# Kernel tuning notes

Hardware: AMD Instinct MI355X
Metric: run time of the kernel (lower is better)

The kernel has to match this reference:

```python
import jax, jax.numpy as jnp
import numpy as np

DILATIONS = (1, 3, 5)
NUM_HEADS = 2


def _conv(x, w, b, dil=1, pad=0):
    # x: [B,C,H,W], w: [O,I,kh,kw] (OIHW), 'same'-style padding = dilation for k=3
    y = jax.lax.conv_general_dilated(
        x, w, window_strides=(1, 1), padding=[(pad, pad), (pad, pad)],
        rhs_dilation=(dil, dil), dimension_numbers=('NCHW', 'OIHW', 'NCHW'))
    return y + b[None, :, None, None]


def setup_inputs() -> dict:
    key = jax.random.key(0)
    ks = jax.random.split(key, 4)
    B, Cin, H, W = 4, 256, 64, 64
    Cout = 256
    x = jax.random.normal(ks[0], (B, Cin, H, W), dtype=jnp.float32)
    # kaiming-uniform-like init scale
    q_w = jax.random.uniform(ks[1], (Cout, Cin, 3, 3), dtype=jnp.float32,
                             minval=-1.0, maxval=1.0) * np.sqrt(6.0 / (Cin * 9))
    k_w = jax.random.uniform(ks[2], (Cout, Cin, 1, 1), dtype=jnp.float32,
                             minval=-1.0, maxval=1.0) * np.sqrt(6.0 / Cin)
    v_w = jax.random.uniform(ks[3], (Cout, Cin, 1, 1), dtype=jnp.float32,
                             minval=-1.0, maxval=1.0) * np.sqrt(6.0 / Cin)
    q_b = jnp.zeros((Cout,), jnp.float32)
    k_b = jnp.zeros((Cout,), jnp.float32)
    v_b = jnp.zeros((Cout,), jnp.float32)
    return {"x": x, "q_w": q_w, "q_b": q_b, "k_w": k_w, "k_b": k_b,
            "v_w": v_w, "v_b": v_b}


def reference(x, q_w, q_b, k_w, k_b, v_w, v_b):
    B, C, H, W = x.shape
    Cout = q_w.shape[0]
    hd = Cout // NUM_HEADS  # head_dim
    # ds_conv2d: sum of SiLU(dilated conv) over dilations 1,3,5 (padding=dilation)
    q = sum(jax.nn.silu(_conv(x, q_w, q_b, dil=d, pad=d)) for d in DILATIONS)
    k = _conv(x, k_w, k_b)
    v = _conv(x, v_w, v_b)
    N = H * W
    # [B, heads, head_dim, N]
    q = q.reshape(B, NUM_HEADS, hd, N)
    k = k.reshape(B, NUM_HEADS, hd, N)
    v = v.reshape(B, NUM_HEADS, hd, N)
    # energy[b,h,n,m] = sum_d q[b,h,d,n] * k[b,h,d,m]
    energy = jnp.einsum('bhdn,bhdm->bhnm', q, k)
    attn = jax.nn.softmax(energy / jnp.sqrt(jnp.float32(hd)), axis=-1)
    # out[b,h,n,d] = sum_m attn[b,h,n,m] * v[b,h,d,m]; then back to [B,C,H,W]
    out = jnp.einsum('bhnm,bhdm->bhdn', attn, v)
    return out.reshape(B, Cout, H, W)
```

## Files before the change

### kernel.cpp

```cpp
#include <hip/hip_runtime.h>
#include <cstdint>

typedef __attribute__((ext_vector_type(8))) _Float16 f16x8;
typedef __attribute__((ext_vector_type(4))) float f32x4;

#define DEV static __device__ __forceinline__

DEV void gld_lds16(void* lds_base, const void* gsrc) {
  __builtin_amdgcn_global_load_lds(
      (const __attribute__((address_space(1))) unsigned int*)gsrc,
      (__attribute__((address_space(3))) unsigned int*)lds_base,
      16, 0, 0);
}
DEV unsigned short f2h(float f) {
  _Float16 h = (_Float16)f;
  return __builtin_bit_cast(unsigned short, h);
}
DEV float h2f(unsigned short u) {
  _Float16 h = __builtin_bit_cast(_Float16, u);
  return (float)h;
}
DEV unsigned pk2h(float a, float b) {
  auto h2 = __builtin_amdgcn_cvt_pkrtz(a, b);
  return __builtin_bit_cast(unsigned, h2);
}
DEV float v_exp2(float x) { float r; asm("v_exp_f32 %0, %1" : "=v"(r) : "v"(x)); return r; }
DEV float v_rcp(float x) { float r; asm("v_rcp_f32 %0, %1" : "=v"(r) : "v"(x)); return r; }


__global__ __launch_bounds__(256) void k_prep_x(const float* __restrict__ x, char* __restrict__ xpad) {
  __shared__ float xs[32 * 257];
  int h = blockIdx.x, b = blockIdx.y, t = threadIdx.x;
  const float* xb = x + (size_t)b * 1048576 + h * 64;
  for (int half = 0; half < 2; half++) {
    int w0 = half * 32;
    for (int kk = 0; kk < 32; kk++) {
      int flat = kk * 256 + t;
      int ci = flat >> 5, w = flat & 31;
      xs[w * 257 + ci] = xb[ci * 4096 + w0 + w];
    }
    __syncthreads();
    for (int g = 0; g < 4; g++) {
      int w = g * 8 + (t >> 5);
      int cg = t & 31;
      float v0 = xs[w * 257 + cg * 8 + 0], v1 = xs[w * 257 + cg * 8 + 1];
      float v2 = xs[w * 257 + cg * 8 + 2], v3 = xs[w * 257 + cg * 8 + 3];
      float v4 = xs[w * 257 + cg * 8 + 4], v5 = xs[w * 257 + cg * 8 + 5];
      float v6 = xs[w * 257 + cg * 8 + 6], v7 = xs[w * 257 + cg * 8 + 7];
      uint4 pk;
      pk.x = pk2h(v0, v1);
      pk.y = pk2h(v2, v3);
      pk.z = pk2h(v4, v5);
      pk.w = pk2h(v6, v7);
      *(uint4*)(xpad + ((size_t)((b * 74 + h + 5) * 74) + w0 + w + 5) * 512 + cg * 16) = pk;
    }
    __syncthreads();
  }
}

__global__ __launch_bounds__(256) void k_prep_w(
    const float* __restrict__ qw, const float* __restrict__ kw, const float* __restrict__ vw,
    unsigned short* __restrict__ Wq, unsigned short* __restrict__ Wk, unsigned short* __restrict__ Wv) {
  int gid = blockIdx.x * 256 + threadIdx.x;
  const float* q9 = qw + (size_t)gid * 9;
#pragma unroll
  for (int tp = 0; tp < 9; tp++) Wq[tp * 65536 + gid] = f2h(q9[tp]);
  Wk[gid] = f2h(kw[gid]);
  Wv[gid] = f2h(vw[gid]);
}

__global__ __launch_bounds__(256, 2) void k_conv_kv(
    const char* __restrict__ xpad, const unsigned short* __restrict__ Wk,
    const unsigned short* __restrict__ Wv, const float* __restrict__ kb,
    const float* __restrict__ vb, unsigned short* __restrict__ K, unsigned short* __restrict__ V) {
  __shared__ char sm[32768];
  char* Xs = sm;
  char* Ws = sm + 16384;
  int t = threadIdx.x, lane = t & 63, wid = t >> 6, q4 = lane >> 4, l15 = lane & 15;
  int px0 = blockIdx.x * 128;
  int b = px0 >> 12, nn = px0 & 4095;
  int h = blockIdx.y;
  int mode = blockIdx.z;
  int co0 = h * 128;
  const char* Wsrc = (const char*)(mode ? Wv : Wk);
  int wm = wid & 1, wn = wid >> 1;
  f32x4 acc[4][4] = {};
  for (int c = 0; c < 4; c++) {
    __syncthreads();
    for (int ch = wid * 1024; ch < 16384; ch += 4096) {
      int o = ch + lane * 16;
      int r = o >> 7;
      int n = nn + r, hh = n >> 6, ww2 = n & 63;
      int col = (o & 127) ^ ((r & 7) << 4);
      gld_lds16(Xs + ch, xpad + ((size_t)((b * 74 + hh + 5) * 74) + ww2 + 5) * 512 + c * 128 + col);
    }
    for (int ch = wid * 1024; ch < 16384; ch += 4096) {
      int o = ch + lane * 16;
      int r = o >> 7;
      int col = (o & 127) ^ ((r & 7) << 4);
      gld_lds16(Ws + ch, Wsrc + (co0 + r) * 512 + c * 128 + col);
    }
    asm volatile("s_waitcnt vmcnt(0)" ::: "memory");
    __syncthreads();
    int xg = mode ? wn : wm;
    int wg = mode ? wm : wn;
#pragma unroll
    for (int kt = 0; kt < 2; kt++) {
      f16x8 xf[4], wf[4];
#pragma unroll
      for (int i = 0; i < 4; i++) {
        int rx = xg * 64 + i * 16 + l15;
        xf[i] = *(const f16x8*)(Xs + ((rx * 128 + kt * 64 + q4 * 16) ^ ((rx & 7) << 4)));
        int rw = wg * 64 + i * 16 + l15;
        wf[i] = *(const f16x8*)(Ws + ((rw * 128 + kt * 64 + q4 * 16) ^ ((rw & 7) << 4)));
      }
#pragma unroll
      for (int m = 0; m < 4; m++)
#pragma unroll
        for (int n = 0; n < 4; n++)
          acc[m][n] = mode ? __builtin_amdgcn_mfma_f32_16x16x32_f16(wf[m], xf[n], acc[m][n], 0, 0, 0)
                           : __builtin_amdgcn_mfma_f32_16x16x32_f16(xf[m], wf[n], acc[m][n], 0, 0, 0);
    }
  }
  int bh = b * 2 + h;
  if (mode == 0) {
#pragma unroll
    for (int m = 0; m < 4; m++)
#pragma unroll
      for (int n = 0; n < 4; n++) {
        int dd = wn * 64 + n * 16 + l15;
        float bias = kb[co0 + dd];
#pragma unroll
        for (int j = 0; j < 4; j++) {
          int npix = nn + wm * 64 + m * 16 + q4 * 4 + j;
          K[(size_t)(bh * 4096 + npix) * 128 + dd] = f2h(acc[m][n][j] + bias);
        }
      }
  } else {
#pragma unroll
    for (int m = 0; m < 4; m++)
#pragma unroll
      for (int j = 0; j < 4; j++) {
        int cr = wm * 64 + m * 16 + q4 * 4 + j;
        float bias = vb[co0 + cr];
#pragma unroll
        for (int n = 0; n < 4; n++) {
          int pc = nn + wn * 64 + (n >> 1) * 32 + (l15 >> 2) * 8 + (n & 1) * 4 + (l15 & 3);
          V[(size_t)(bh * 128 + cr) * 4096 + pc] = f2h(acc[m][n][j] + bias);
        }
      }
  }
}

__global__ __launch_bounds__(512, 2) void k_conv_q(
    const char* __restrict__ xpad, const unsigned short* __restrict__ Wq,
    const float* __restrict__ qb, unsigned short* __restrict__ Q) {
  extern __shared__ char sm[];
  char* As = sm + 32768;
  int t = threadIdx.x, lane = t & 63, wid = t >> 6, q4 = lane >> 4, l15 = lane & 15;
  int fblk = blockIdx.x;
  int g = (fblk & 7) * 32 + (fblk >> 3);
  int h2 = g & 31, b = (g >> 5) & 3, ch2 = g >> 7;
  int h0 = h2 * 2;
  int co0 = ch2 * 128;
  int wn = wid & 1, wq = wid >> 1;
  int hr = wq >> 1, wloc = wq & 1;
  const int dil[3] = {1, 3, 5};
  const char* WqB = (const char*)Wq;
  f32x4 accd[3][2][4] = {};

#define STAGE_B(dstbuf, kh_, c_, kw_)                                             \
  {                                                                               \
    const char* src_ = WqB + (size_t)((kh_)*3 + (kw_)) * 131072 + co0 * 512 + (c_)*128; \
    char* dst_ = (dstbuf);                                                        \
    for (int ch = wid * 1024; ch < 16384; ch += 8192) {                           \
      int o = ch + lane * 16;                                                     \
      int r = o >> 7;                                                             \
      int col = (o & 127) ^ ((r & 7) << 4);                                       \
      gld_lds16(dst_ + ch, src_ + r * 512 + col);                                 \
    }                                                                             \
  }

#define STAGE_A_ROW(slot_, pr_, c_)                                               \
  {                                                                               \
    const char* src_ = xpad + ((size_t)(b * 74 + (pr_)) * 74) * 512 + (c_)*128;   \
    char* dst_ = As + (slot_)*9472;                                               \
    for (int ch = wid * 1024; ch < 9472; ch += 8192) {                            \
      int o = ch + lane * 16;                                                     \
      if (o < 9472) {                                                             \
        int r = o >> 7;                                                           \
        int col = (o & 127) ^ ((r & 7) << 4);                                     \
        gld_lds16(dst_ + ch, src_ + r * 512 + col);                               \
      }                                                                           \
    }                                                                             \
  }

#define STAGE_A(kh_, c_)                                                          \
  {                                                                               \
    if ((kh_) == 1) {                                                             \
      for (int s = 0; s < 2; s++) STAGE_A_ROW(s, h0 + s + 5, c_);                 \
    } else {                                                                      \
      for (int di = 0; di < 3; di++)                                              \
        for (int s = 0; s < 2; s++)                                               \
          STAGE_A_ROW(di * 2 + s, h0 + s + ((kh_)-1) * dil[di] + 5, c_);          \
    }                                                                             \
  }

  STAGE_A(0, 0);
  STAGE_B(sm, 0, 0, 0);
  asm volatile("s_waitcnt vmcnt(0)" ::: "memory");
  __syncthreads();

  int cur = 0;
  for (int kh = 0; kh < 3; kh++) {
    for (int c = 0; c < 4; c++) {
      for (int kw = 0; kw < 3; kw++) {
        int kwn = kw + 1, cn = c, khn = kh;
        if (kwn == 3) { kwn = 0; cn = c + 1; if (cn == 4) { cn = 0; khn = kh + 1; } }
        char* Bnext = cur ? sm : sm + 16384;
        if (khn < 3) STAGE_B(Bnext, khn, cn, kwn);
        const char* Bc = cur ? sm + 16384 : sm;
        f16x8 bf[4][2];
#pragma unroll
        for (int n = 0; n < 4; n++)
#pragma unroll
          for (int kt = 0; kt < 2; kt++) {
            int rc = wn * 64 + n * 16 + l15;
            bf[n][kt] = *(const f16x8*)(Bc + ((rc * 128 + kt * 64 + q4 * 16) ^ ((rc & 7) << 4)));
          }
#pragma unroll
        for (int di = 0; di < 3; di++) {
          int dw = (kw - 1) * dil[di] + 5;
          const char* Ad = As + (kh == 1 ? hr : di * 2 + hr) * 9472;
          f16x8 af[2][2];
#pragma unroll
          for (int m = 0; m < 2; m++)
#pragma unroll
            for (int kt = 0; kt < 2; kt++) {
              int wp = wloc * 32 + m * 16 + l15 + dw;
              af[m][kt] = *(const f16x8*)(Ad + ((wp * 128 + kt * 64 + q4 * 16) ^ ((wp & 7) << 4)));
            }
          __builtin_amdgcn_s_setprio(1);
#pragma unroll
          for (int m = 0; m < 2; m++)
#pragma unroll
            for (int n = 0; n < 4; n++)
#pragma unroll
              for (int kt = 0; kt < 2; kt++)
                accd[di][m][n] = __builtin_amdgcn_mfma_f32_16x16x32_f16(af[m][kt], bf[n][kt], accd[di][m][n], 0, 0, 0);
          __builtin_amdgcn_s_setprio(0);
        }
        asm volatile("s_waitcnt vmcnt(0)" ::: "memory");
        __syncthreads();
        cur ^= 1;
      }
      int cn2 = c + 1, khn2 = kh;
      if (cn2 == 4) { cn2 = 0; khn2 = kh + 1; }
      if (khn2 < 3) {
        STAGE_A(khn2, cn2);
        asm volatile("s_waitcnt vmcnt(0)" ::: "memory");
        __syncthreads();
      }
    }
  }
#undef STAGE_A
#undef STAGE_A_ROW
#undef STAGE_B
  const float LOG2E = 1.4426950408889634f;
  const float QSCALE = 0.12751879523176862f;
#pragma unroll
  for (int n = 0; n < 4; n++) {
    float bias = qb[co0 + wn * 64 + n * 16 + l15];
#pragma unroll
    for (int m = 0; m < 2; m++)
#pragma unroll
      for (int j = 0; j < 4; j++) {
        float s = 0.f;
#pragma unroll
        for (int di = 0; di < 3; di++) {
          float v = accd[di][m][n][j] + bias;
          s += v * v_rcp(1.0f + v_exp2(-v * LOG2E));
        }
        int w = wloc * 32 + m * 16 + q4 * 4 + j;
        int npix = (h0 + hr) * 64 + w;
        int dd = wn * 64 + n * 16 + l15;
        Q[((size_t)(b * 2 + ch2) * 4096 + npix) * 128 + dd] = f2h(s * QSCALE);
      }
  }
}

__global__ __launch_bounds__(256, 2) void k_attn(
    const unsigned short* __restrict__ Q, const unsigned short* __restrict__ K,
    const unsigned short* __restrict__ V, float* __restrict__ out,
    unsigned short* __restrict__ o1buf, float* __restrict__ mlbuf) {
  __shared__ char sm[65536];
  int t = threadIdx.x, lane = t & 63, wid = t >> 6, q4 = lane >> 4, l15 = lane & 15;
  int fblk = blockIdx.x;
  int g = (fblk & 7) * 64 + (fblk >> 3);
  int nb = g & 31, bh = (g >> 5) & 7, half = g >> 8;
  int b = bh >> 1, hh = bh & 1;
  int n0 = nb * 128;
  const char* Qg = (const char*)(Q + ((size_t)bh * 4096 + n0) * 128);
  const char* Kg = (const char*)(K + (size_t)bh * 4096 * 128) + half * 524288;
  const char* Vg = (const char*)(V + (size_t)bh * 128 * 4096) + half * 4096;
  f16x8 qf[2][4];
#pragma unroll
  for (int nt = 0; nt < 2; nt++)
#pragma unroll
    for (int kt = 0; kt < 4; kt++) {
      int rn = wid * 32 + nt * 16 + l15;
      qf[nt][kt] = *(const f16x8*)(Qg + (size_t)rn * 256 + kt * 64 + q4 * 16);
    }
  const char* pT0 = sm + (((l15 * 256 + 0 * 64 + q4 * 16) ^ (l15 << 4)));
  const char* pT1 = sm + (((l15 * 256 + 1 * 64 + q4 * 16) ^ (l15 << 4)));
  const char* pT2 = sm + (((l15 * 256 + 2 * 64 + q4 * 16) ^ (l15 << 4)));
  const char* pT3 = sm + (((l15 * 256 + 3 * 64 + q4 * 16) ^ (l15 << 4)));
  const char* pU0 = sm + 32768 + (((l15 * 128 + 0 * 64 + q4 * 16) ^ ((l15 & 7) << 4)));
  const char* pU1 = sm + 32768 + (((l15 * 128 + 1 * 64 + q4 * 16) ^ ((l15 & 7) << 4)));
  int ks[4], vs[4], lch[4];
#pragma unroll
  for (int c2 = 0; c2 < 4; c2++) {
    int ch = wid * 1024 + c2 * 4096;
    int o = ch + lane * 16;
    lch[c2] = ch;
    ks[c2] = o ^ (((o >> 8) & 15) << 4);
    int dd = o >> 7;
    vs[c2] = dd * 8192 + ((o & 127) ^ ((dd & 7) << 4));
  }
#pragma unroll
  for (int c2 = 0; c2 < 4; c2++) gld_lds16(sm + lch[c2], Kg + ks[c2]);
#pragma unroll
  for (int c2 = 0; c2 < 4; c2++) gld_lds16(sm + 32768 + lch[c2], Vg + vs[c2]);
  asm volatile("s_waitcnt vmcnt(0)" ::: "memory");
  __syncthreads();
  f32x4 Ofr[8][2] = {};
  float mrun[2] = {-3e38f, -3e38f};
  float lrun[2] = {0.f, 0.f};
  const char* kgp = Kg;
  const char* vgp = Vg;

#define ATTN_ITER(KB, VB, KBN, VBN, do_pf)                                          \
  {                                                                                 \
    if (do_pf) {                                                                    \
      kgp += 16384;                                                                 \
      vgp += 128;                                                                   \
      _Pragma("unroll") for (int c2 = 0; c2 < 4; c2++)                              \
          gld_lds16(sm + (KBN) + lch[c2], kgp + ks[c2]);                            \
      _Pragma("unroll") for (int c2 = 0; c2 < 4; c2++)                              \
          gld_lds16(sm + (VBN) + lch[c2], vgp + vs[c2]);                            \
    }                                                                               \
    f32x4 sT[4][2] = {};                                                            \
    _Pragma("unroll") for (int kt = 0; kt < 4; kt++) {                              \
      const char* pT = (kt == 0) ? pT0 : (kt == 1) ? pT1 : (kt == 2) ? pT2 : pT3;   \
      f16x8 kf[4];                                                                  \
      _Pragma("unroll") for (int mt = 0; mt < 4; mt++)                              \
          kf[mt] = *(const f16x8*)(pT + (KB) + mt * 4096);                          \
      __builtin_amdgcn_s_setprio(1);                                                \
      _Pragma("unroll") for (int mt = 0; mt < 4; mt++)                              \
          _Pragma("unroll") for (int nt = 0; nt < 2; nt++)                          \
              sT[mt][nt] = __builtin_amdgcn_mfma_f32_16x16x32_f16(                  \
                  kf[mt], qf[nt][kt], sT[mt][nt], 0, 0, 0);                         \
      __builtin_amdgcn_s_setprio(0);                                                \
    }                                                                               \
    unsigned U[2][4][2];                                                            \
    _Pragma("unroll") for (int nt = 0; nt < 2; nt++) {                              \
      float mx = sT[0][nt][0];                                                      \
      _Pragma("unroll") for (int mt = 0; mt < 4; mt++)                              \
          _Pragma("unroll") for (int j = 0; j < 4; j++) mx = fmaxf(mx, sT[mt][nt][j]); \
      mx = fmaxf(mx, __shfl_xor(mx, 16));                                           \
      mx = fmaxf(mx, __shfl_xor(mx, 32));                                           \
      float mn = mrun[nt];                                                          \
      if (!__all(mx - mn <= 8.f)) {                                                 \
        mn = fmaxf(mrun[nt], mx);                                                   \
        float al = v_exp2(mrun[nt] - mn);                                           \
        mrun[nt] = mn;                                                              \
        lrun[nt] *= al;                                                             \
        _Pragma("unroll") for (int dt = 0; dt < 8; dt++) Ofr[dt][nt] *= al;         \
      }                                                                             \
      float rs = 0.f;                                                               \
      _Pragma("unroll") for (int mt = 0; mt < 4; mt++) {                            \
        float p0 = v_exp2(sT[mt][nt][0] - mn);                                      \
        float p1 = v_exp2(sT[mt][nt][1] - mn);                                      \
        float p2 = v_exp2(sT[mt][nt][2] - mn);                                      \
        float p3 = v_exp2(sT[mt][nt][3] - mn);                                      \
        rs += (p0 + p1) + (p2 + p3);                                                \
        U[nt][mt][0] = pk2h(p0, p1);                                                \
        U[nt][mt][1] = pk2h(p2, p3);                                                \
      }                                                                             \
      rs += __shfl_xor(rs, 16);                                                     \
      rs += __shfl_xor(rs, 32);                                                     \
      lrun[nt] += rs;                                                               \
    }                                                                               \
    _Pragma("unroll") for (int kt = 0; kt < 2; kt++) {                              \
      const char* pU = kt ? pU1 : pU0;                                              \
      f16x8 pf[2];                                                                  \
      _Pragma("unroll") for (int nt = 0; nt < 2; nt++) {                            \
        uint4 fr;                                                                   \
        fr.x = U[nt][2 * kt][0];                                                    \
        fr.y = U[nt][2 * kt][1];                                                    \
        fr.z = U[nt][2 * kt + 1][0];                                                \
        fr.w = U[nt][2 * kt + 1][1];                                                \
        pf[nt] = __builtin_bit_cast(f16x8, fr);                                     \
      }                                                                             \
      f16x8 vf[8];                                                                  \
      _Pragma("unroll") for (int dt = 0; dt < 8; dt++)                              \
          vf[dt] = *(const f16x8*)(pU + ((VB)-32768) + dt * 2048);                  \
      __builtin_amdgcn_s_setprio(1);                                                \
      _Pragma("unroll") for (int dt = 0; dt < 8; dt++)                              \
          _Pragma("unroll") for (int nt = 0; nt < 2; nt++)                          \
              Ofr[dt][nt] = __builtin_amdgcn_mfma_f32_16x16x32_f16(                 \
                  vf[dt], pf[nt], Ofr[dt][nt], 0, 0, 0);                            \
      __builtin_amdgcn_s_setprio(0);                                                \
    }                                                                               \
    __syncthreads();                                                                \
  }

  for (int it2 = 0; it2 < 16; it2++) {
    ATTN_ITER(0, 32768, 16384, 49152, true);
    ATTN_ITER(16384, 49152, 0, 32768, (it2 < 15));
  }
#undef ATTN_ITER

  if (q4 == 0) {
#pragma unroll
    for (int nt = 0; nt < 2; nt++) {
      int n = n0 + wid * 32 + nt * 16 + l15;
      float2 ml;
      ml.x = mrun[nt];
      ml.y = lrun[nt];
      *(float2*)(mlbuf + ((size_t)(half * 8 + bh) * 4096 + n) * 2) = ml;
    }
  }
  if (half == 0) {
    float* og = out + (size_t)(b * 256 + hh * 128) * 4096 + n0 + wid * 32;
#pragma unroll
    for (int dt = 0; dt < 8; dt++)
#pragma unroll
      for (int nt = 0; nt < 2; nt++)
#pragma unroll
        for (int j = 0; j < 4; j++) {
          int dd = dt * 16 + q4 * 4 + j;
          og[(size_t)dd * 4096 + nt * 16 + l15] = Ofr[dt][nt][j];
        }
  } else {
    float li[2] = {v_rcp(lrun[0]), v_rcp(lrun[1])};
    unsigned short* og = o1buf + (size_t)bh * 128 * 4096 + n0 + wid * 32;
#pragma unroll
    for (int dt = 0; dt < 8; dt++)
#pragma unroll
      for (int nt = 0; nt < 2; nt++)
#pragma unroll
        for (int j = 0; j < 4; j++) {
          int dd = dt * 16 + q4 * 4 + j;
          og[(size_t)dd * 4096 + nt * 16 + l15] = f2h(Ofr[dt][nt][j] * li[nt]);
        }
  }
}

__global__ __launch_bounds__(256) void k_combine(
    float* __restrict__ out, const unsigned short* __restrict__ o1,
    const float* __restrict__ ml) {
  int tid = blockIdx.x * 256 + threadIdx.x;
  int n = tid & 4095, dg = (tid >> 12) & 7, bh = tid >> 15;
  float2 ml0 = *(const float2*)(ml + ((size_t)bh * 4096 + n) * 2);
  float2 ml1 = *(const float2*)(ml + ((size_t)(8 + bh) * 4096 + n) * 2);
  float ms = fmaxf(ml0.x, ml1.x);
  float a0 = v_exp2(ml0.x - ms);
  float w1 = ml1.y * v_exp2(ml1.x - ms);
  float inv = 1.f / (ml0.y * a0 + w1);
  size_t ob = ((size_t)((bh >> 1) * 256 + (bh & 1) * 128 + dg * 16)) * 4096 + n;
  size_t o1b = ((size_t)(bh * 128 + dg * 16)) * 4096 + n;
#pragma unroll 4
  for (int j = 0; j < 16; j++) {
    float v0 = out[ob + (size_t)j * 4096];
    float v1 = h2f(o1[o1b + (size_t)j * 4096]);
    out[ob + (size_t)j * 4096] = (v0 * a0 + v1 * w1) * inv;
  }
}

extern "C" void kernel_launch(void* const* d_in, const int* in_sizes, int n_in,
                              void* d_out, int out_size, void* d_ws, size_t ws_size,
                              hipStream_t stream) {
  (void)in_sizes; (void)n_in; (void)out_size;
  const float* x  = (const float*)d_in[0];
  const float* qw = (const float*)d_in[1];
  const float* qb = (const float*)d_in[2];
  const float* kw = (const float*)d_in[3];
  const float* kb = (const float*)d_in[4];
  const float* vw = (const float*)d_in[5];
  const float* vb = (const float*)d_in[6];
  char* ws = (char*)d_ws;
  if (ws_size < 37822464) return;
  char* xpad = ws;
  unsigned short* Wq = (unsigned short*)(ws + 11214848);
  unsigned short* Wk = (unsigned short*)(ws + 12394496);
  unsigned short* Wv = (unsigned short*)(ws + 12525568);
  unsigned short* Qb = (unsigned short*)(ws + 12656640);
  unsigned short* Kb = (unsigned short*)(ws + 21045248);
  unsigned short* Vb = (unsigned short*)(ws + 29433856);
  unsigned short* O1 = (unsigned short*)ws;
  float* ML = (float*)(ws + 11214848);
  hipMemsetAsync(xpad, 0, 11214848, stream);
  k_prep_x<<<dim3(64, 4), dim3(256), 0, stream>>>(x, xpad);
  k_prep_w<<<dim3(256), dim3(256), 0, stream>>>(qw, kw, vw, Wq, Wk, Wv);
  k_conv_kv<<<dim3(128, 2, 2), dim3(256), 0, stream>>>(xpad, Wk, Wv, kb, vb, Kb, Vb);
  k_conv_q<<<dim3(256), dim3(512), 89600, stream>>>(xpad, Wq, qb, Qb);
  k_attn<<<dim3(512), dim3(256), 0, stream>>>(Qb, Kb, Vb, (float*)d_out, O1, ML);
  k_combine<<<dim3(1024), dim3(256), 0, stream>>>((float*)d_out, O1, ML);
}
```

Baseline: 175.3 us.

## Double-buffer conv staging in LDS and fold padding zeroing into prep kernel

The K/V conv kernel now double-buffers its X and W tiles in 64KB of LDS, issuing the next channel chunk's loads before the MFMAs on the current one. The Q conv kernel also double-buffers its activation rows, prefetching the next (kh,c) rows during the first kw step, which removes a separate wait and barrier. The full-workspace memset is replaced by having k_prep_x zero only the padding border of xpad. This raises Q-conv LDS use to 146KB per block, which lowers occupancy, in exchange for hiding load latency and dropping an 11MB memset.

```diff
diff --git a/kernel.cpp b/kernel.cpp
--- a/kernel.cpp
+++ b/kernel.cpp
@@ -31,6 +31,18 @@
 __global__ __launch_bounds__(256) void k_prep_x(const float* __restrict__ x, char* __restrict__ xpad) {
   __shared__ float xs[32 * 257];
   int h = blockIdx.x, b = blockIdx.y, t = threadIdx.x;
+  uint4 z = {0, 0, 0, 0};
+  char* rowbase = xpad + ((size_t)(b * 74 + h + 5) * 74) * 512;
+  for (int i = t; i < 320; i += 256) {
+    int col = i >> 5, off = (i & 31) * 16;
+    int w = (col < 5) ? col : 64 + col;
+    *(uint4*)(rowbase + (size_t)w * 512 + off) = z;
+  }
+  if (h < 10) {
+    int r = (h < 5) ? h : 64 + h;
+    char* rb = xpad + ((size_t)(b * 74 + r) * 74) * 512;
+    for (int i = t; i < 2368; i += 256) *(uint4*)(rb + (size_t)i * 16) = z;
+  }
   const float* xb = x + (size_t)b * 1048576 + h * 64;
   for (int half = 0; half < 2; half++) {
     int w0 = half * 32;
@@ -73,9 +85,7 @@
     const char* __restrict__ xpad, const unsigned short* __restrict__ Wk,
     const unsigned short* __restrict__ Wv, const float* __restrict__ kb,
     const float* __restrict__ vb, unsigned short* __restrict__ K, unsigned short* __restrict__ V) {
-  __shared__ char sm[32768];
-  char* Xs = sm;
-  char* Ws = sm + 16384;
+  __shared__ char sm[65536];
   int t = threadIdx.x, lane = t & 63, wid = t >> 6, q4 = lane >> 4, l15 = lane & 15;
   int px0 = blockIdx.x * 128;
   int b = px0 >> 12, nn = px0 & 4095;
@@ -84,24 +94,35 @@
   int co0 = h * 128;
   const char* Wsrc = (const char*)(mode ? Wv : Wk);
   int wm = wid & 1, wn = wid >> 1;
+
+#define STAGE_KV(base_, c_)                                                       \
+  {                                                                               \
+    for (int ch = wid * 1024; ch < 16384; ch += 4096) {                           \
+      int o = ch + lane * 16;                                                     \
+      int r = o >> 7;                                                             \
+      int n = nn + r, hh = n >> 6, ww2 = n & 63;                                  \
+      int col = (o & 127) ^ ((r & 7) << 4);                                       \
+      gld_lds16((base_) + ch,                                                     \
+                xpad + ((size_t)((b * 74 + hh + 5) * 74) + ww2 + 5) * 512 + (c_)*128 + col); \
+    }                                                                             \
+    for (int ch = wid * 1024; ch < 16384; ch += 4096) {                           \
+      int o = ch + lane * 16;                                                     \
+      int r = o >> 7;                                                             \
+      int col = (o & 127) ^ ((r & 7) << 4);                                       \
+      gld_lds16((base_) + 16384 + ch, Wsrc + (co0 + r) * 512 + (c_)*128 + col);   \
+    }                                                                             \
+  }
+
+  STAGE_KV(sm, 0);
+  asm volatile("s_waitcnt vmcnt(0)" ::: "memory");
+  __syncthreads();
+
   f32x4 acc[4][4] = {};
   for (int c = 0; c < 4; c++) {
-    __syncthreads();
-    for (int ch = wid * 1024; ch < 16384; ch += 4096) {
-      int o = ch + lane * 16;
-      int r = o >> 7;
-      int n = nn + r, hh = n >> 6, ww2 = n & 63;
-      int col = (o & 127) ^ ((r & 7) << 4);
-      gld_lds16(Xs + ch, xpad + ((size_t)((b * 74 + hh + 5) * 74) + ww2 + 5) * 512 + c * 128 + col);
-    }
-    for (int ch = wid * 1024; ch < 16384; ch += 4096) {
-      int o = ch + lane * 16;
-      int r = o >> 7;
-      int col = (o & 127) ^ ((r & 7) << 4);
-      gld_lds16(Ws + ch, Wsrc + (co0 + r) * 512 + c * 128 + col);
-    }
-    asm volatile("s_waitcnt vmcnt(0)" ::: "memory");
-    __syncthreads();
+    char* cb = sm + (c & 1) * 32768;
+    if (c < 3) STAGE_KV(sm + ((c & 1) ^ 1) * 32768, c + 1);
+    const char* Xs = cb;
+    const char* Ws = cb + 16384;
     int xg = mode ? wn : wm;
     int wg = mode ? wm : wn;
 #pragma unroll
@@ -121,7 +142,10 @@
           acc[m][n] = mode ? __builtin_amdgcn_mfma_f32_16x16x32_f16(wf[m], xf[n], acc[m][n], 0, 0, 0)
                            : __builtin_amdgcn_mfma_f32_16x16x32_f16(xf[m], wf[n], acc[m][n], 0, 0, 0);
     }
-  }
+    asm volatile("s_waitcnt vmcnt(0)" ::: "memory");
+    __syncthreads();
+  }
+#undef STAGE_KV
   int bh = b * 2 + h;
   if (mode == 0) {
 #pragma unroll
@@ -156,7 +180,6 @@
     const char* __restrict__ xpad, const unsigned short* __restrict__ Wq,
     const float* __restrict__ qb, unsigned short* __restrict__ Q) {
   extern __shared__ char sm[];
-  char* As = sm + 32768;
   int t = threadIdx.x, lane = t & 63, wid = t >> 6, q4 = lane >> 4, l15 = lane & 15;
   int fblk = blockIdx.x;
   int g = (fblk & 7) * 32 + (fblk >> 3);
@@ -181,10 +204,10 @@
     }                                                                             \
   }
 
-#define STAGE_A_ROW(slot_, pr_, c_)                                               \
+#define STAGE_A_ROW(abase_, slot_, pr_, c_)                                       \
   {                                                                               \
     const char* src_ = xpad + ((size_t)(b * 74 + (pr_)) * 74) * 512 + (c_)*128;   \
-    char* dst_ = As + (slot_)*9472;                                               \
+    char* dst_ = (abase_) + (slot_)*9472;                                         \
     for (int ch = wid * 1024; ch < 9472; ch += 8192) {                            \
       int o = ch + lane * 16;                                                     \
       if (o < 9472) {                                                             \
@@ -195,31 +218,35 @@
     }                                                                             \
   }
 
-#define STAGE_A(kh_, c_)                                                          \
+#define STAGE_A(abase_, kh_, c_)                                                  \
   {                                                                               \
     if ((kh_) == 1) {                                                             \
-      for (int s = 0; s < 2; s++) STAGE_A_ROW(s, h0 + s + 5, c_);                 \
+      for (int s = 0; s < 2; s++) STAGE_A_ROW(abase_, s, h0 + s + 5, c_);         \
     } else {                                                                      \
       for (int di = 0; di < 3; di++)                                              \
         for (int s = 0; s < 2; s++)                                               \
-          STAGE_A_ROW(di * 2 + s, h0 + s + ((kh_)-1) * dil[di] + 5, c_);          \
+          STAGE_A_ROW(abase_, di * 2 + s, h0 + s + ((kh_)-1) * dil[di] + 5, c_);  \
     }                                                                             \
   }
 
-  STAGE_A(0, 0);
+  STAGE_A(sm + 32768, 0, 0);
   STAGE_B(sm, 0, 0, 0);
   asm volatile("s_waitcnt vmcnt(0)" ::: "memory");
   __syncthreads();
 
-  int cur = 0;
+  int curB = 0, curA = 0;
   for (int kh = 0; kh < 3; kh++) {
     for (int c = 0; c < 4; c++) {
+      int cn2 = c + 1, khn2 = kh;
+      if (cn2 == 4) { cn2 = 0; khn2 = kh + 1; }
       for (int kw = 0; kw < 3; kw++) {
         int kwn = kw + 1, cn = c, khn = kh;
         if (kwn == 3) { kwn = 0; cn = c + 1; if (cn == 4) { cn = 0; khn = kh + 1; } }
-        char* Bnext = cur ? sm : sm + 16384;
+        char* Bnext = curB ? sm : sm + 16384;
         if (khn < 3) STAGE_B(Bnext, khn, cn, kwn);
-        const char* Bc = cur ? sm + 16384 : sm;
+        if (kw == 0 && khn2 < 3) STAGE_A(sm + 32768 + (curA ^ 1) * 56832, khn2, cn2);
+        const char* Bc = curB ? sm + 16384 : sm;
+        const char* Abase = sm + 32768 + curA * 56832;
         f16x8 bf[4][2];
 #pragma unroll
         for (int n = 0; n < 4; n++)
@@ -231,7 +258,7 @@
 #pragma unroll
         for (int di = 0; di < 3; di++) {
           int dw = (kw - 1) * dil[di] + 5;
-          const char* Ad = As + (kh == 1 ? hr : di * 2 + hr) * 9472;
+          const char* Ad = Abase + (kh == 1 ? hr : di * 2 + hr) * 9472;
           f16x8 af[2][2];
 #pragma unroll
           for (int m = 0; m < 2; m++)
@@ -252,15 +279,9 @@
         }
         asm volatile("s_waitcnt vmcnt(0)" ::: "memory");
         __syncthreads();
-        cur ^= 1;
+        curB ^= 1;
       }
-      int cn2 = c + 1, khn2 = kh;
-      if (cn2 == 4) { cn2 = 0; khn2 = kh + 1; }
-      if (khn2 < 3) {
-        STAGE_A(khn2, cn2);
-        asm volatile("s_waitcnt vmcnt(0)" ::: "memory");
-        __syncthreads();
-      }
+      if (khn2 < 3) curA ^= 1;
     }
   }
 #undef STAGE_A
@@ -500,11 +521,10 @@
   unsigned short* Vb = (unsigned short*)(ws + 29433856);
   unsigned short* O1 = (unsigned short*)ws;
   float* ML = (float*)(ws + 11214848);
-  hipMemsetAsync(xpad, 0, 11214848, stream);
   k_prep_x<<<dim3(64, 4), dim3(256), 0, stream>>>(x, xpad);
   k_prep_w<<<dim3(256), dim3(256), 0, stream>>>(qw, kw, vw, Wq, Wk, Wv);
   k_conv_kv<<<dim3(128, 2, 2), dim3(256), 0, stream>>>(xpad, Wk, Wv, kb, vb, Kb, Vb);
-  k_conv_q<<<dim3(256), dim3(512), 89600, stream>>>(xpad, Wq, qb, Qb);
+  k_conv_q<<<dim3(256), dim3(512), 146432, stream>>>(xpad, Wq, qb, Qb);
   k_attn<<<dim3(512), dim3(256), 0, stream>>>(Qb, Kb, Vb, (float*)d_out, O1, ML);
   k_combine<<<dim3(1024), dim3(256), 0, stream>>>((float*)d_out, O1, ML);
 }
```

Measured after the change: 166.3 us. 5.1% less time.
